# Kernel tuning notes

Measured on AMD Instinct MI355X. Metric: run time of the kernel, lower is better.

Reference implementation:

```python
import jax, jax.numpy as jnp
import numpy as np

N = 100000
E = 3200000
F_IN = 512
H = 128
C = 40


def gcn_conv(x, edge_index, edge_weight, W, b):
    """PyG GCNConv: x' = D^-1/2 (A+I) D^-1/2 (x W) + b, symmetric norm with self-loops."""
    n = x.shape[0]
    x = x @ W  # [N, H]
    row, col = edge_index[0], edge_index[1]
    sl = jnp.arange(n)
    row_f = jnp.concatenate([row, sl])
    col_f = jnp.concatenate([col, sl])
    w_f = jnp.concatenate([edge_weight, jnp.ones((n,), x.dtype)])
    deg = jax.ops.segment_sum(w_f, col_f, num_segments=n)  # in-degree incl. self-loop
    dinv = jnp.where(deg > 0, jax.lax.rsqrt(deg), 0.0)
    norm = dinv[row_f] * w_f * dinv[col_f]  # [E+N]
    msg = x[row_f] * norm[:, None]          # gather + scale
    out = jax.ops.segment_sum(msg, col_f, num_segments=n)  # scatter-add to targets
    return out + b


def setup_inputs() -> dict:
    key = jax.random.key(0)
    ks = jax.random.split(key, 12)
    inp = {
        "x": jax.random.normal(ks[0], (N, F_IN), jnp.float32),
        "edge_index": jax.random.randint(ks[1], (2, E), 0, N, jnp.int64),
        "edge_weight": jax.random.uniform(ks[2], (E,), jnp.float32),
        # first_lin
        "W1": jax.random.normal(ks[3], (F_IN, H), jnp.float32) / np.sqrt(F_IN),
        "b1": jnp.zeros((H,), jnp.float32),
        # conv layers (num_layers=2)
        "Wc1": jax.random.normal(ks[4], (H, H), jnp.float32) / np.sqrt(H),
        "bc1": jnp.zeros((H,), jnp.float32),
        "Wc2": jax.random.normal(ks[5], (H, H), jnp.float32) / np.sqrt(H),
        "bc2": jnp.zeros((H,), jnp.float32),
        # lin2
        "W2": jax.random.normal(ks[6], (H, C), jnp.float32) / np.sqrt(H),
        "b2": jnp.zeros((C,), jnp.float32),
        # wide layer
        "Ww": jax.random.normal(ks[7], (F_IN, C), jnp.float32) / np.sqrt(F_IN),
        "bw": jnp.zeros((C,), jnp.float32),
        # attention layer (-> 2 logits per node)
        "Wa": jax.random.normal(ks[8], (F_IN, 2), jnp.float32) / np.sqrt(F_IN),
        "ba": jnp.zeros((2,), jnp.float32),
    }
    return inp


def reference(x, edge_index, edge_weight, W1, b1, Wc1, bc1, Wc2, bc2, W2, b2, Ww, bw, Wa, ba):
    # deep branch (res_type=0.0, eval mode: dropout = identity)
    h = jax.nn.relu(x @ W1 + b1)
    h = jax.nn.relu(gcn_conv(h, edge_index, edge_weight, Wc1, bc1))
    h = jax.nn.relu(gcn_conv(h, edge_index, edge_weight, Wc2, bc2))
    deep_x = h @ W2 + b2  # [N, C]
    # wide branch on raw features
    wide_x = x @ Ww + bw  # [N, C]
    # attention fusion: softmax over 2 branch logits per node
    attn = jax.nn.softmax(x @ Wa + ba, axis=-1)  # [N, 2]
    out = deep_x * attn[:, 0:1] + wide_x * attn[:, 1:2]
    return out
```

## Files before the change

kernel.cpp:

```cpp
#include <hip/hip_runtime.h>
#include <hip/hip_bf16.h>
#include <cstdint>

#define N_NODES 100000
#define N_EDGES 3200000

typedef __attribute__((ext_vector_type(8))) short short8;
typedef __attribute__((ext_vector_type(4))) float floatx4;

#define FXS 8388608.0f
#define EA 320
#define EPB 10000
#define NBKT 391

__device__ __forceinline__ unsigned short f2bf(float f) {
    unsigned u = __float_as_uint(f);
    u += 0x7fff + ((u >> 16) & 1);
    return (unsigned short)(u >> 16);
}
__device__ __forceinline__ float bf2f(unsigned short s) {
    return __uint_as_float(((unsigned)s) << 16);
}
__device__ __forceinline__ float bflo(unsigned u) {
    return __uint_as_float(u << 16);
}
__device__ __forceinline__ float bfhi(unsigned u) {
    return __uint_as_float(u & 0xffff0000u);
}
__device__ __forceinline__ unsigned pack_bf2(float a, float b) {
    union { __hip_bfloat162 h2; unsigned u; } cv;
    cv.h2 = __float22bfloat162_rn(make_float2(a, b));
    return cv.u;
}

__global__ void setup_misc(const float* __restrict__ W1, const float* __restrict__ b1,
                           const float* __restrict__ Ww, const float* __restrict__ bw,
                           const float* __restrict__ Wa, const float* __restrict__ ba,
                           const float* __restrict__ Wc1, const float* __restrict__ Wc2,
                           const float* __restrict__ W2,
                           unsigned short* __restrict__ WcatT, float* __restrict__ bcat,
                           unsigned short* __restrict__ Wc1T, unsigned short* __restrict__ Wc2T,
                           unsigned short* __restrict__ W2T) {
    int bid = blockIdx.x, tid = threadIdx.x;
    if (bid < 192) {
        int c = bid;
        for (int kk = tid; kk < 512; kk += 256) {
            float v;
            if (c < 128)      v = W1[kk * 128 + c];
            else if (c < 168) v = Ww[kk * 40 + (c - 128)];
            else if (c < 170) v = Wa[kk * 2 + (c - 168)];
            else              v = 0.f;
            WcatT[(size_t)c * 512 + kk] = f2bf(v);
        }
        if (tid == 0) {
            float b;
            if (c < 128)      b = b1[c];
            else if (c < 168) b = bw[c - 128];
            else if (c < 170) b = ba[c - 168];
            else              b = 0.f;
            bcat[c] = b;
        }
    } else if (bid < 320) {
        int c = bid - 192;
        if (tid < 128) Wc1T[(size_t)c * 128 + tid] = f2bf(Wc1[tid * 128 + c]);
        else { int k = tid - 128; Wc2T[(size_t)c * 128 + k] = f2bf(Wc2[k * 128 + c]); }
    } else {
        int c = bid - 320;
        if (tid < 128)
            W2T[(size_t)c * 128 + tid] = (c < 40) ? f2bf(W2[tid * 40 + c])
                                                  : (unsigned short)0;
    }
}

template <int EPI, int NT, int AF32>
__device__ __forceinline__ void gemm_body(
    int mblk, const void* __restrict__ Avoid, const unsigned short* __restrict__ BT,
    int M, int K,
    unsigned short* __restrict__ C0, float* __restrict__ C1, float* __restrict__ C2,
    const float* __restrict__ bias, const float* __restrict__ rowscale) {
    constexpr int NB = 32 * NT;
    constexpr int RB = NT / 2;
    __shared__ __align__(16) unsigned short Ast[64 * 40];
    __shared__ __align__(16) unsigned short Bst[NB * 40];

    int tid = threadIdx.x;
    int m0 = mblk * 64;
    int wave = tid >> 6, lane = tid & 63;
    int quad = lane >> 4, mi = lane & 15;
    int wm = (wave >> 1) * 32;
    int wn = (wave & 1) * (16 * NT);

    int srow = tid >> 2;
    int sk8 = (tid & 3) * 8;

    int arow = m0 + srow; if (arow >= M) arow = M - 1;

    const float* Afp = (const float*)Avoid + (size_t)arow * K + sk8;
    const unsigned short* Abp = (const unsigned short*)Avoid + (size_t)arow * K + sk8;
    int brow[RB], bk8[RB];
    const unsigned short* Bp[RB];
#pragma unroll
    for (int r = 0; r < RB; ++r) {
        int i = tid + r * 256;
        brow[r] = i >> 2;
        bk8[r] = (i & 3) * 8;
        Bp[r] = BT + (size_t)(i >> 2) * K + (i & 3) * 8;
    }

    float4 fA0, fA1; uint4 aR;
    if (AF32) { fA0 = *(const float4*)(Afp); fA1 = *(const float4*)(Afp + 4); }
    else      { aR = *(const uint4*)(Abp); }
    uint4 bR[RB];
#pragma unroll
    for (int r = 0; r < RB; ++r) bR[r] = *(const uint4*)(Bp[r]);

    floatx4 acc[2][NT] = {};

    for (int kc = 0; kc < K; kc += 32) {
        if (AF32) {
            uint4 pk;
            pk.x = pack_bf2(fA0.x, fA0.y);
            pk.y = pack_bf2(fA0.z, fA0.w);
            pk.z = pack_bf2(fA1.x, fA1.y);
            pk.w = pack_bf2(fA1.z, fA1.w);
            *(uint4*)&Ast[srow * 40 + sk8] = pk;
        } else {
            *(uint4*)&Ast[srow * 40 + sk8] = aR;
        }
#pragma unroll
        for (int r = 0; r < RB; ++r)
            *(uint4*)&Bst[brow[r] * 40 + bk8[r]] = bR[r];
        __syncthreads();

        if (kc + 32 < K) {
            if (AF32) {
                fA0 = *(const float4*)(Afp + kc + 32);
                fA1 = *(const float4*)(Afp + kc + 36);
            } else {
                aR = *(const uint4*)(Abp + kc + 32);
            }
#pragma unroll
            for (int r = 0; r < RB; ++r) bR[r] = *(const uint4*)(Bp[r] + kc + 32);
        }

        short8 a0 = *(const short8*)&Ast[(wm + mi) * 40 + quad * 8];
        short8 a1 = *(const short8*)&Ast[(wm + 16 + mi) * 40 + quad * 8];
#pragma unroll
        for (int nt = 0; nt < NT; ++nt) {
            short8 b = *(const short8*)&Bst[(wn + nt * 16 + mi) * 40 + quad * 8];
            acc[0][nt] = __builtin_amdgcn_mfma_f32_16x16x32_bf16(a0, b, acc[0][nt], 0, 0, 0);
            acc[1][nt] = __builtin_amdgcn_mfma_f32_16x16x32_bf16(a1, b, acc[1][nt], 0, 0, 0);
        }
        __syncthreads();
    }

#pragma unroll
    for (int mt = 0; mt < 2; ++mt) {
#pragma unroll
        for (int nt = 0; nt < NT; ++nt) {
            floatx4 v = acc[mt][nt];
            int gn = wn + nt * 16 + mi;
#pragma unroll
            for (int r = 0; r < 4; ++r) {
                int gm = m0 + wm + mt * 16 + quad * 4 + r;
                if (gm >= M) continue;
                float val = v[r];
                if (EPI == 0) {
                    C0[(size_t)gm * 128 + gn] = f2bf(rowscale[gm] * val);
                } else if (EPI == 1) {
                    val += bias[gn];
                    if (gn < 128)      C0[(size_t)gm * 128 + gn] = f2bf(fmaxf(val, 0.f));
                    else if (gn < 168) C1[(size_t)gm * 40 + (gn - 128)] = val;
                    else if (gn < 170) C2[(size_t)gm * 2 + (gn - 168)] = val;
                } else {
                    if (gn < 40) {
                        float l0 = rowscale[gm * 2], l1 = rowscale[gm * 2 + 1];
                        float mx = fmaxf(l0, l1);
                        float e0 = __expf(l0 - mx), e1 = __expf(l1 - mx);
                        float inv = 1.f / (e0 + e1);
                        C1[(size_t)gm * 40 + gn] =
                            (val + bias[gn]) * (e0 * inv) +
                            C2[(size_t)gm * 40 + gn] * (e1 * inv);
                    }
                }
            }
        }
    }
}

__global__ __launch_bounds__(256) void megaA(
    const float* __restrict__ x, const unsigned short* __restrict__ WcatT,
    unsigned short* __restrict__ h0, float* __restrict__ wide, float* __restrict__ attnL,
    const float* __restrict__ bcat, const int* __restrict__ ei,
    int* __restrict__ histA, int M, int e) {
    int bid = blockIdx.x;
    if (bid >= EA) {
        gemm_body<1, 6, 1>(bid - EA, x, WcatT, M, 512, h0, wide, attnL, bcat, nullptr);
        return;
    }
    __shared__ unsigned lh[NBKT];
    int tid = threadIdx.x;
    for (int i = tid; i < NBKT; i += 256) lh[i] = 0;
    __syncthreads();
    int base = bid * EPB, end = base + EPB; if (end > e) end = e;
    for (int i = base + tid; i < end; i += 256) {
        int d = ei[e + i];
        atomicAdd(&lh[d >> 8], 1u);
    }
    __syncthreads();
    for (int k = tid; k < NBKT; k += 256) histA[k * EA + bid] = (int)lh[k];
}

__global__ __launch_bounds__(256) void scatterA(
    const int* __restrict__ ei, const float* __restrict__ ew,
    const int* __restrict__ offA, uint2* __restrict__ cs, int e) {
    int bid = blockIdx.x, tid = threadIdx.x;
    __shared__ unsigned lh[NBKT];
    __shared__ int lo[NBKT];
    for (int i = tid; i < NBKT; i += 256) { lh[i] = 0; lo[i] = offA[i * EA + bid]; }
    __syncthreads();
    int base = bid * EPB, end = base + EPB; if (end > e) end = e;
    for (int i = base + tid; i < end; i += 256) {
        int d = ei[e + i];
        int r = ei[i];
        float w = ew[i];
        int k = d >> 8;
        unsigned lr = atomicAdd(&lh[k], 1u);
        cs[lo[k] + (int)lr] = make_uint2((unsigned)r | ((unsigned)(d & 255) << 24),
                                         __float_as_uint(w));
    }
}

__global__ __launch_bounds__(1024) void passB1(
    const uint2* __restrict__ cs, const int* __restrict__ offA,
    int* __restrict__ ptr, float* __restrict__ dinv, int n, int e) {
    int k = blockIdx.x, tid = threadIdx.x;
    __shared__ unsigned lc[256], lw[256];
    __shared__ int ls[256];
    if (tid < 256) { lc[tid] = 0; lw[tid] = 0; }
    __syncthreads();
    int start = offA[k * EA];
    int end = (k == NBKT - 1) ? e : offA[(k + 1) * EA];
    for (int i = start + tid; i < end; i += 1024) {
        uint2 u = cs[i];
        int dlow = u.x >> 24;
        unsigned fx = (unsigned)(__uint_as_float(u.y) * FXS);
        atomicAdd(&lc[dlow], 1u);
        atomicAdd(&lw[dlow], fx);
    }
    __syncthreads();
    int v = (tid < 256) ? (int)lc[tid] : 0;
    if (tid < 256) ls[tid] = v;
    __syncthreads();
    for (int off = 1; off < 256; off <<= 1) {
        int t = (tid < 256 && tid >= off) ? ls[tid - off] : 0;
        __syncthreads();
        if (tid < 256) ls[tid] += t;
        __syncthreads();
    }
    if (tid < 256) {
        int d = (k << 8) + tid;
        if (d < n) {
            ptr[d]  = start + ls[tid] - v;
            dinv[d] = rsqrtf(1.0f + (float)lw[tid] * (1.0f / FXS));
        }
    }
    if (k == NBKT - 1 && tid == 0) ptr[n] = e;
}

__global__ __launch_bounds__(256) void megaB(
    const unsigned short* __restrict__ h0, const unsigned short* __restrict__ Wc1T,
    unsigned short* __restrict__ tmpB, const float* __restrict__ dinv,
    const uint2* __restrict__ cs, const int* __restrict__ offA,
    const int* __restrict__ ptr, uint2* __restrict__ edges, int M, int n, int e) {
    int bid = blockIdx.x;
    if (bid >= NBKT) {
        gemm_body<0, 4, 0>(bid - NBKT, h0, Wc1T, M, 128, tmpB, nullptr, nullptr, nullptr, dinv);
        return;
    }
    int k = bid, tid = threadIdx.x;
    __shared__ unsigned lc[256];
    __shared__ int lp[256];
    { lc[tid] = 0; int d = (k << 8) + tid; lp[tid] = (d < n) ? ptr[d] : 0; }
    __syncthreads();
    int start = offA[k * EA];
    int end = (k == NBKT - 1) ? e : offA[(k + 1) * EA];
    for (int i = start + tid; i < end; i += 256) {
        uint2 u = cs[i];
        int dlow = u.x >> 24;
        unsigned src = u.x & 0x00FFFFFFu;
        unsigned lr = atomicAdd(&lc[dlow], 1u);
        edges[lp[dlow] + (int)lr] = make_uint2(src, u.y);
    }
}

__global__ __launch_bounds__(256) void gemm_conv(
    const unsigned short* __restrict__ A, const unsigned short* __restrict__ BT,
    unsigned short* __restrict__ C0, const float* __restrict__ rowscale, int M) {
    gemm_body<0, 4, 0>(blockIdx.x, A, BT, M, 128, C0, nullptr, nullptr, nullptr, rowscale);
}

__global__ __launch_bounds__(256) void gemm_final(
    const unsigned short* __restrict__ A, const unsigned short* __restrict__ W2T,
    float* __restrict__ out, float* __restrict__ wide,
    const float* __restrict__ attnL, const float* __restrict__ b2, int M) {
    gemm_body<2, 2, 0>(blockIdx.x, A, W2T, M, 128, nullptr, out, wide, b2, attnL);
}

__global__ void scan1(const int* __restrict__ in, int* __restrict__ out,
                      int* __restrict__ bsum, int n) {
    __shared__ int s[1024];
    int tid = threadIdx.x;
    int i = blockIdx.x * 1024 + tid;
    int v = (i < n) ? in[i] : 0;
    s[tid] = v;
    __syncthreads();
    for (int off = 1; off < 1024; off <<= 1) {
        int t = (tid >= off) ? s[tid - off] : 0;
        __syncthreads();
        s[tid] += t;
        __syncthreads();
    }
    if (i < n) out[i] = s[tid] - v;
    if (tid == 1023) bsum[blockIdx.x] = s[1023];
}

__global__ void scan_bsums(int* bsum, int nb) {
    __shared__ int s[1024];
    int tid = threadIdx.x;
    int v = (tid < nb) ? bsum[tid] : 0;
    s[tid] = v;
    __syncthreads();
    for (int off = 1; off < 1024; off <<= 1) {
        int t = (tid >= off) ? s[tid - off] : 0;
        __syncthreads();
        s[tid] += t;
        __syncthreads();
    }
    if (tid < nb) bsum[tid] = s[tid] - v;
}

__global__ void scan_add(int* __restrict__ out, const int* __restrict__ bsum,
                         int n, int tailv) {
    int i = blockIdx.x * 1024 + threadIdx.x;
    if (i < n) out[i] += bsum[blockIdx.x];
    if (i == 0 && tailv >= 0) out[n] = tailv;
}

__global__ __launch_bounds__(256) void propagate(
    const unsigned int* __restrict__ tmp2,
    unsigned int* __restrict__ out2,
    const float* __restrict__ bias, const float* __restrict__ dinv,
    const int* __restrict__ ptr, const uint2* __restrict__ edges, int n) {
    int wave = threadIdx.x >> 6, lane = threadIdx.x & 63;
    int d = blockIdx.x * 4 + wave;
    if (d >= n) return;

    unsigned u = tmp2[(size_t)d * 64 + lane];
    float acc0 = bflo(u);
    float acc1 = bfhi(u);

    int p = ptr[d], p1 = ptr[d + 1];
    for (; p + 8 <= p1; p += 8) {
        uint2 q[8];
#pragma unroll
        for (int j = 0; j < 8; ++j) q[j] = edges[p + j];
        unsigned rv[8];
#pragma unroll
        for (int j = 0; j < 8; ++j) rv[j] = tmp2[(size_t)q[j].x * 64 + lane];
#pragma unroll
        for (int j = 0; j < 8; ++j) {
            float w = __uint_as_float(q[j].y);
            acc0 += w * bflo(rv[j]); acc1 += w * bfhi(rv[j]);
        }
    }
    for (; p < p1; ++p) {
        uint2 q = edges[p];
        unsigned a = tmp2[(size_t)q.x * 64 + lane];
        float w = __uint_as_float(q.y);
        acc0 += w * bflo(a); acc1 += w * bfhi(a);
    }
    float di = dinv[d];
    float v0 = fmaxf(di * acc0 + bias[2 * lane], 0.f);
    float v1 = fmaxf(di * acc1 + bias[2 * lane + 1], 0.f);
    out2[(size_t)d * 64 + lane] = (unsigned)f2bf(v0) | ((unsigned)f2bf(v1) << 16);
}

extern "C" void kernel_launch(void* const* d_in, const int* in_sizes, int n_in,
                              void* d_out, int out_size, void* d_ws, size_t ws_size,
                              hipStream_t stream) {
    (void)in_sizes; (void)n_in; (void)out_size; (void)ws_size;
    const float* x   = (const float*)d_in[0];
    const int*   ei  = (const int*)d_in[1];
    const float* ew  = (const float*)d_in[2];
    const float* W1  = (const float*)d_in[3];
    const float* b1  = (const float*)d_in[4];
    const float* Wc1 = (const float*)d_in[5];
    const float* bc1 = (const float*)d_in[6];
    const float* Wc2 = (const float*)d_in[7];
    const float* bc2 = (const float*)d_in[8];
    const float* W2  = (const float*)d_in[9];
    const float* b2  = (const float*)d_in[10];
    const float* Ww  = (const float*)d_in[11];
    const float* bw  = (const float*)d_in[12];
    const float* Wa  = (const float*)d_in[13];
    const float* ba  = (const float*)d_in[14];
    float* out = (float*)d_out;

    const int N = N_NODES, E = N_EDGES;
    char* ws = (char*)d_ws;
    size_t off = 0;
    auto alloc = [&](size_t bytes) -> void* {
        void* p = ws + off;
        off = (off + bytes + 255) & ~(size_t)255;
        return p;
    };
    unsigned short* bufA = (unsigned short*)alloc((size_t)N * 128 * 2);
    unsigned short* bufB = (unsigned short*)alloc((size_t)N * 128 * 2);
    float* wide  = (float*)alloc((size_t)N * 40 * 4);
    float* attnL = (float*)alloc((size_t)N * 2 * 4);
    float* dinv  = (float*)alloc((size_t)N * 4);
    int*   histA = (int*)alloc((size_t)NBKT * EA * 4);
    uint2* cs    = (uint2*)alloc((size_t)E * 8);
    int*   ptr   = (int*)alloc((size_t)(N + 1) * 4);
    int*   bsum  = (int*)alloc(1024 * 4);
    uint2* edges = (uint2*)alloc((size_t)E * 8);
    unsigned short* WcatT = (unsigned short*)alloc((size_t)192 * 512 * 2);
    unsigned short* Wc1T  = (unsigned short*)alloc((size_t)128 * 128 * 2);
    unsigned short* Wc2T  = (unsigned short*)alloc((size_t)128 * 128 * 2);
    unsigned short* W2T   = (unsigned short*)alloc((size_t)64 * 128 * 2);
    float* bcat  = (float*)alloc(192 * 4);

    const int MB = (N + 63) / 64;
    const int NHA = NBKT * EA;

    setup_misc<<<384, 256, 0, stream>>>(W1, b1, Ww, bw, Wa, ba, Wc1, Wc2, W2,
                                        WcatT, bcat, Wc1T, Wc2T, W2T);

    megaA<<<EA + MB, 256, 0, stream>>>(x, WcatT, bufA, wide, attnL, bcat,
                                       ei, histA, N, E);

    int nbA = (NHA + 1023) / 1024;
    scan1<<<nbA, 1024, 0, stream>>>(histA, histA, bsum, NHA);
    scan_bsums<<<1, 1024, 0, stream>>>(bsum, nbA);
    scan_add<<<nbA, 1024, 0, stream>>>(histA, bsum, NHA, -1);

    scatterA<<<EA, 256, 0, stream>>>(ei, ew, histA, cs, E);

    passB1<<<NBKT, 1024, 0, stream>>>(cs, histA, ptr, dinv, N, E);

    megaB<<<NBKT + MB, 256, 0, stream>>>(bufA, Wc1T, bufB, dinv,
                                         cs, histA, ptr, edges, N, N, E);
    propagate<<<(N + 3) / 4, 256, 0, stream>>>((const unsigned int*)bufB, (unsigned int*)bufA,
                                               bc1, dinv, ptr, edges, N);

    gemm_conv<<<MB, 256, 0, stream>>>(bufA, Wc2T, bufB, dinv, N);
    propagate<<<(N + 3) / 4, 256, 0, stream>>>((const unsigned int*)bufB, (unsigned int*)bufA,
                                               bc2, dinv, ptr, edges, N);

    gemm_final<<<MB, 256, 0, stream>>>(bufA, W2T, out, wide, attnL, b2, N);
}
```

Measured before the change: 839.8 us.

## Double-buffer A tile in LDS and load B fragments directly from global

The GEMM body now double-buffers the A tile in shared memory, so each k-step needs one barrier instead of two. B fragments are read straight from global memory (L2/L1-cached) into registers in MFMA layout, which drops the B shared-memory staging. This cuts LDS traffic and synchronization. The cost is that B is re-read by every wave without coalesced staging, which could add global/L2 load latency.

```diff
diff --git a/kernel.cpp b/kernel.cpp
--- a/kernel.cpp
+++ b/kernel.cpp
@@ -78,10 +78,7 @@
     int M, int K,
     unsigned short* __restrict__ C0, float* __restrict__ C1, float* __restrict__ C2,
     const float* __restrict__ bias, const float* __restrict__ rowscale) {
-    constexpr int NB = 32 * NT;
-    constexpr int RB = NT / 2;
-    __shared__ __align__(16) unsigned short Ast[64 * 40];
-    __shared__ __align__(16) unsigned short Bst[NB * 40];
+    __shared__ __align__(16) unsigned short Ast[2][64 * 40];
 
     int tid = threadIdx.x;
     int m0 = mblk * 64;
@@ -97,61 +94,61 @@
 
     const float* Afp = (const float*)Avoid + (size_t)arow * K + sk8;
     const unsigned short* Abp = (const unsigned short*)Avoid + (size_t)arow * K + sk8;
-    int brow[RB], bk8[RB];
-    const unsigned short* Bp[RB];
-#pragma unroll
-    for (int r = 0; r < RB; ++r) {
-        int i = tid + r * 256;
-        brow[r] = i >> 2;
-        bk8[r] = (i & 3) * 8;
-        Bp[r] = BT + (size_t)(i >> 2) * K + (i & 3) * 8;
-    }
-
-    float4 fA0, fA1; uint4 aR;
-    if (AF32) { fA0 = *(const float4*)(Afp); fA1 = *(const float4*)(Afp + 4); }
-    else      { aR = *(const uint4*)(Abp); }
-    uint4 bR[RB];
-#pragma unroll
-    for (int r = 0; r < RB; ++r) bR[r] = *(const uint4*)(Bp[r]);
+    const unsigned short* Bfp = BT + (size_t)(wn + mi) * K + quad * 8;
+
+    {
+        if (AF32) {
+            float4 f0 = *(const float4*)(Afp);
+            float4 f1 = *(const float4*)(Afp + 4);
+            uint4 pk;
+            pk.x = pack_bf2(f0.x, f0.y); pk.y = pack_bf2(f0.z, f0.w);
+            pk.z = pack_bf2(f1.x, f1.y); pk.w = pack_bf2(f1.z, f1.w);
+            *(uint4*)&Ast[0][srow * 40 + sk8] = pk;
+        } else {
+            *(uint4*)&Ast[0][srow * 40 + sk8] = *(const uint4*)(Abp);
+        }
+    }
+    __syncthreads();
 
     floatx4 acc[2][NT] = {};
 
+    int cur = 0;
     for (int kc = 0; kc < K; kc += 32) {
-        if (AF32) {
-            uint4 pk;
-            pk.x = pack_bf2(fA0.x, fA0.y);
-            pk.y = pack_bf2(fA0.z, fA0.w);
-            pk.z = pack_bf2(fA1.x, fA1.y);
-            pk.w = pack_bf2(fA1.z, fA1.w);
-            *(uint4*)&Ast[srow * 40 + sk8] = pk;
-        } else {
-            *(uint4*)&Ast[srow * 40 + sk8] = aR;
-        }
-#pragma unroll
-        for (int r = 0; r < RB; ++r)
-            *(uint4*)&Bst[brow[r] * 40 + bk8[r]] = bR[r];
-        __syncthreads();
-
-        if (kc + 32 < K) {
+        bool more = (kc + 32 < K);
+        float4 fA0, fA1; uint4 aR;
+        if (more) {
             if (AF32) {
                 fA0 = *(const float4*)(Afp + kc + 32);
                 fA1 = *(const float4*)(Afp + kc + 36);
             } else {
                 aR = *(const uint4*)(Abp + kc + 32);
             }
-#pragma unroll
-            for (int r = 0; r < RB; ++r) bR[r] = *(const uint4*)(Bp[r] + kc + 32);
-        }
-
-        short8 a0 = *(const short8*)&Ast[(wm + mi) * 40 + quad * 8];
-        short8 a1 = *(const short8*)&Ast[(wm + 16 + mi) * 40 + quad * 8];
+        }
+        uint4 bv[NT];
+#pragma unroll
+        for (int nt = 0; nt < NT; ++nt)
+            bv[nt] = *(const uint4*)(Bfp + (size_t)nt * 16 * K + kc);
+
+        short8 a0 = *(const short8*)&Ast[cur][(wm + mi) * 40 + quad * 8];
+        short8 a1 = *(const short8*)&Ast[cur][(wm + 16 + mi) * 40 + quad * 8];
 #pragma unroll
         for (int nt = 0; nt < NT; ++nt) {
-            short8 b = *(const short8*)&Bst[(wn + nt * 16 + mi) * 40 + quad * 8];
+            short8 b = *(const short8*)&bv[nt];
             acc[0][nt] = __builtin_amdgcn_mfma_f32_16x16x32_bf16(a0, b, acc[0][nt], 0, 0, 0);
             acc[1][nt] = __builtin_amdgcn_mfma_f32_16x16x32_bf16(a1, b, acc[1][nt], 0, 0, 0);
         }
-        __syncthreads();
+        if (more) {
+            if (AF32) {
+                uint4 pk;
+                pk.x = pack_bf2(fA0.x, fA0.y); pk.y = pack_bf2(fA0.z, fA0.w);
+                pk.z = pack_bf2(fA1.x, fA1.y); pk.w = pack_bf2(fA1.z, fA1.w);
+                *(uint4*)&Ast[cur ^ 1][srow * 40 + sk8] = pk;
+            } else {
+                *(uint4*)&Ast[cur ^ 1][srow * 40 + sk8] = aR;
+            }
+            __syncthreads();
+            cur ^= 1;
+        }
     }
 
 #pragma unroll
```

After: 781.2 us. 7.0% less time.
